# Kernel optimization log

Hardware: AMD Instinct MI355X
Metric: run time of the kernel (lower is better)

Reference implementation:

```python
import jax, jax.numpy as jnp
import numpy as np

# Coefficients expressing each of the 16 soft binary logic gates as
# c0 + ca*a + cb*b + cab*(a*b), in standard difflogic op order:
# 0:False 1:AND 2:a&~b 3:A 4:~a&b 5:B 6:XOR 7:OR 8:NOR 9:XNOR
# 10:~B 11:B=>A 12:~A 13:A=>B 14:NAND 15:True
GATE_COEF = jnp.array([
    [0, 0, 0, 0],
    [0, 0, 0, 1],
    [0, 1, 0, -1],
    [0, 1, 0, 0],
    [0, 0, 1, -1],
    [0, 0, 1, 0],
    [0, 1, 1, -2],
    [0, 1, 1, -1],
    [1, -1, -1, 1],
    [1, -1, -1, 2],
    [1, 0, -1, 0],
    [1, 0, -1, 1],
    [1, -1, 0, 0],
    [1, -1, 0, 1],
    [1, 0, 0, -1],
    [1, 0, 0, 0],
], dtype=jnp.float32)  # [16, 4]

INPUT_DIM = 8192
HIDDEN_DIMS = [16384, 16384, 16384, 16384]
OUTPUT_DIM = 1000
BATCH = 2048
TAU = 1.0
N_GATES = 16


def setup_inputs() -> dict:
    key = jax.random.key(0)
    kx, key = jax.random.split(key)
    inp = {"x": jax.random.uniform(kx, (BATCH, INPUT_DIM), dtype=jnp.float32)}
    dims = [INPUT_DIM] + HIDDEN_DIMS + [OUTPUT_DIM]
    for i in range(len(dims) - 1):
        in_d, out_d = dims[i], dims[i + 1]
        kw, ka, kb, key = jax.random.split(key, 4)
        inp[f"w{i}"] = jax.random.normal(kw, (out_d, N_GATES), dtype=jnp.float32)
        inp[f"ia{i}"] = jax.random.randint(ka, (out_d,), 0, in_d, dtype=jnp.int32)
        inp[f"ib{i}"] = jax.random.randint(kb, (out_d,), 0, in_d, dtype=jnp.int32)
    return inp


def _logic_layer(x, w, ia, ib):
    # gather the two inputs of every neuron: [batch, out_dim]
    a = x[:, ia]
    b = x[:, ib]
    p = jax.nn.softmax(w, axis=-1)              # [out_dim, 16]
    coef = p @ GATE_COEF                         # [out_dim, 4]
    # weighted mixture of all 16 gates, fused via bilinear form
    return coef[:, 0] + coef[:, 1] * a + coef[:, 2] * b + coef[:, 3] * (a * b)


def reference(x, w0, w1, w2, w3, w4, ia0, ia1, ia2, ia3, ia4, ib0, ib1, ib2, ib3, ib4):
    ws = [w0, w1, w2, w3, w4]
    ias = [ia0, ia1, ia2, ia3, ia4]
    ibs = [ib0, ib1, ib2, ib3, ib4]
    h = x
    for w, ia, ib in zip(ws, ias, ibs):
        h = _logic_layer(h, w, ia, ib)
    # GroupSum(output_dim, tau): split last dim into output_dim groups, sum, /tau
    batch = h.shape[0]
    group = h.shape[-1] // OUTPUT_DIM
    out = h.reshape(batch, OUTPUT_DIM, group).sum(-1) / TAU
    return out
```

## Files before the change

kernel.cpp:

```cpp
#include <hip/hip_runtime.h>


#define NBATCH 2048
#define IN_DIM 8192
#define HID 16384
#define OUT_DIM 1000
#define LDS_ENT 32768
#define MARKV 0x7FFFFFFF

typedef __attribute__((ext_vector_type(4))) _Float16 half4;
typedef __attribute__((ext_vector_type(2))) _Float16 half2v;

__device__ __constant__ float GC_dev[64] = {
    0, 0, 0, 0,   0, 0, 0, 1,   0, 1, 0, -1,  0, 1, 0, 0,
    0, 0, 1, -1,  0, 0, 1, 0,   0, 1, 1, -2,  0, 1, 1, -1,
    1, -1, -1, 1, 1, -1, -1, 2, 1, 0, -1, 0,  1, 0, -1, 1,
    1, -1, 0, 0,  1, -1, 0, 1,  1, 0, 0, -1,  1, 0, 0, 0
};

struct Tabs {
    const float* w[5];
    const int* ia[5];
    const int* ib[5];
};

__global__ __launch_bounds__(256) void coef_kernel(Tabs args, half4* __restrict__ coefFull) {
    int g = blockIdx.x * 256 + threadIdx.x;
    int l = g >> 14;
    int j = g & (HID - 1);
    if (l == 4 && j >= OUT_DIM) return;

    const float4* w4 = (const float4*)(args.w[l] + (size_t)j * 16);
    float v[16];
#pragma unroll
    for (int i = 0; i < 4; ++i) {
        float4 t = w4[i];
        v[4*i+0] = t.x; v[4*i+1] = t.y; v[4*i+2] = t.z; v[4*i+3] = t.w;
    }
    float m = v[0];
#pragma unroll
    for (int g2 = 1; g2 < 16; ++g2) m = fmaxf(m, v[g2]);
    float s = 0.f;
#pragma unroll
    for (int g2 = 0; g2 < 16; ++g2) { v[g2] = __expf(v[g2] - m); s += v[g2]; }
    float inv = 1.f / s;
    float c0 = 0.f, c1 = 0.f, c2 = 0.f, c3 = 0.f;
#pragma unroll
    for (int g2 = 0; g2 < 16; ++g2) {
        c0 += v[g2] * GC_dev[g2*4+0];
        c1 += v[g2] * GC_dev[g2*4+1];
        c2 += v[g2] * GC_dev[g2*4+2];
        c3 += v[g2] * GC_dev[g2*4+3];
    }
    half4 c;
    c[0] = (_Float16)(c0*inv); c[1] = (_Float16)(c1*inv);
    c[2] = (_Float16)(c2*inv); c[3] = (_Float16)(c3*inv);
    coefFull[g] = c;
}

__global__ __launch_bounds__(1024) void build_kernel(
    Tabs args, const half4* __restrict__ coefFull,
    unsigned int* __restrict__ tabIdx, half4* __restrict__ tabCoef,
    int* __restrict__ header) {
    __shared__ int mapA[HID];
    __shared__ int mapB[HID];
    __shared__ int cnt;
    const int t = threadIdx.x;

    for (int i = t; i < HID; i += 1024) mapA[i] = -1;
    if (t == 0) cnt = 0;
    __syncthreads();
    if (t < OUT_DIM) { mapA[args.ia[4][t]] = MARKV; mapA[args.ib[4][t]] = MARKV; }
    __syncthreads();
    for (int i = t; i < HID; i += 1024)
        if (mapA[i] == MARKV) mapA[i] = atomicAdd(&cnt, 1);
    __syncthreads();
    const int count3 = cnt;
    if (t < OUT_DIM) {
        unsigned a = (unsigned)(LDS_ENT - count3 + mapA[args.ia[4][t]]);
        unsigned b = (unsigned)(LDS_ENT - count3 + mapA[args.ib[4][t]]);
        tabIdx[4*HID + t] = a | (b << 16);
        tabCoef[4*HID + t] = coefFull[4*HID + t];
    }
    __syncthreads();

    for (int i = t; i < HID; i += 1024) mapB[i] = -1;
    if (t == 0) cnt = 0;
    __syncthreads();
    for (int i = t; i < HID; i += 1024)
        if (mapA[i] >= 0) { mapB[args.ia[3][i]] = MARKV; mapB[args.ib[3][i]] = MARKV; }
    __syncthreads();
    for (int i = t; i < HID; i += 1024)
        if (mapB[i] == MARKV) mapB[i] = atomicAdd(&cnt, 1);
    __syncthreads();
    const int count2 = cnt;
    for (int i = t; i < HID; i += 1024) {
        int s = mapA[i];
        if (s >= 0) {
            unsigned a = 8192u + (unsigned)mapB[args.ia[3][i]];
            unsigned b = 8192u + (unsigned)mapB[args.ib[3][i]];
            tabIdx[3*HID + s] = a | (b << 16);
            tabCoef[3*HID + s] = coefFull[3*HID + i];
        }
    }
    __syncthreads();

    for (int i = t; i < HID; i += 1024) mapA[i] = -1;
    if (t == 0) cnt = 0;
    __syncthreads();
    for (int i = t; i < HID; i += 1024)
        if (mapB[i] >= 0) { mapA[args.ia[2][i]] = MARKV; mapA[args.ib[2][i]] = MARKV; }
    __syncthreads();
    for (int i = t; i < HID; i += 1024)
        if (mapA[i] == MARKV) mapA[i] = atomicAdd(&cnt, 1);
    __syncthreads();
    const int count1 = cnt;
    {
        unsigned base1 = (unsigned)(LDS_ENT - count1);
        for (int i = t; i < HID; i += 1024) {
            int s = mapB[i];
            if (s >= 0) {
                unsigned a = base1 + (unsigned)mapA[args.ia[2][i]];
                unsigned b = base1 + (unsigned)mapA[args.ib[2][i]];
                tabIdx[2*HID + s] = a | (b << 16);
                tabCoef[2*HID + s] = coefFull[2*HID + i];
            }
        }
    }
    __syncthreads();

    for (int i = t; i < HID; i += 1024) mapB[i] = -1;
    if (t == 0) cnt = 0;
    __syncthreads();
    for (int i = t; i < HID; i += 1024)
        if (mapA[i] >= 0) { mapB[args.ia[1][i]] = MARKV; mapB[args.ib[1][i]] = MARKV; }
    __syncthreads();
    for (int i = t; i < HID; i += 1024)
        if (mapB[i] == MARKV) mapB[i] = atomicAdd(&cnt, 1);
    __syncthreads();
    const int count0 = cnt;
    for (int i = t; i < HID; i += 1024) {
        int s = mapA[i];
        if (s >= 0) {
            unsigned a = 8192u + (unsigned)mapB[args.ia[1][i]];
            unsigned b = 8192u + (unsigned)mapB[args.ib[1][i]];
            tabIdx[1*HID + s] = a | (b << 16);
            tabCoef[1*HID + s] = coefFull[1*HID + i];
        }
    }
    __syncthreads();

    for (int i = t; i < HID; i += 1024) {
        int s = mapB[i];
        if (s >= 0) {
            tabIdx[0*HID + s] =
                (unsigned)args.ia[0][i] | ((unsigned)args.ib[0][i] << 16);
            tabCoef[0*HID + s] = coefFull[0*HID + i];
        }
    }
    if (t == 0) {
        header[0] = count0; header[1] = count1;
        header[2] = count2; header[3] = count3;
    }
}

__device__ __forceinline__ void layer_pass(
    half2v* lds, const unsigned* __restrict__ tIdx,
    const half4* __restrict__ tCoef, int n, int wbase, int t) {
    for (int j = t; j < n; j += 1024) {
        unsigned idx = tIdx[j];
        half4 c = tCoef[j];
        half2v pa = lds[idx & 0xFFFFu];
        half2v pb = lds[idx >> 16];
        float c0 = (float)c[0], c1 = (float)c[1];
        float c2 = (float)c[2], c3 = (float)c[3];
        float a0 = (float)pa[0], a1 = (float)pa[1];
        float q0 = (float)pb[0], q1 = (float)pb[1];
        half2v o;
        o[0] = (_Float16)fmaf(fmaf(c3, q0, c1), a0, fmaf(c2, q0, c0));
        o[1] = (_Float16)fmaf(fmaf(c3, q1, c1), a1, fmaf(c2, q1, c0));
        lds[wbase + j] = o;
    }
    __syncthreads();
}

__global__ __launch_bounds__(1024) void fused_kernel(
    const float* __restrict__ x, const unsigned* __restrict__ tabIdx,
    const half4* __restrict__ tabCoef, const int* __restrict__ header,
    float* __restrict__ out) {
    extern __shared__ half2v lds[];
    int bp = blockIdx.x;
    int t = threadIdx.x;
    int b0 = 2 * bp, b1 = 2 * bp + 1;
    int n0 = header[0], n1 = header[1], n2 = header[2], n3 = header[3];

    const float4* xr0 = (const float4*)(x + (size_t)b0 * IN_DIM);
    const float4* xr1 = (const float4*)(x + (size_t)b1 * IN_DIM);
#pragma unroll
    for (int i = 0; i < 2; ++i) {
        int e = i * 1024 + t;
        float4 v0 = xr0[e];
        float4 v1 = xr1[e];
        half2v h0; h0[0] = (_Float16)v0.x; h0[1] = (_Float16)v1.x;
        half2v h1; h1[0] = (_Float16)v0.y; h1[1] = (_Float16)v1.y;
        half2v h2; h2[0] = (_Float16)v0.z; h2[1] = (_Float16)v1.z;
        half2v h3; h3[0] = (_Float16)v0.w; h3[1] = (_Float16)v1.w;
        lds[4*e+0] = h0; lds[4*e+1] = h1; lds[4*e+2] = h2; lds[4*e+3] = h3;
    }
    __syncthreads();

    layer_pass(lds, tabIdx + 0*HID, tabCoef + 0*HID, n0, 8192,          t);
    layer_pass(lds, tabIdx + 1*HID, tabCoef + 1*HID, n1, LDS_ENT - n1, t);
    layer_pass(lds, tabIdx + 2*HID, tabCoef + 2*HID, n2, 8192,          t);
    layer_pass(lds, tabIdx + 3*HID, tabCoef + 3*HID, n3, LDS_ENT - n3, t);

    if (t < OUT_DIM) {
        unsigned idx = tabIdx[4*HID + t];
        half4 c = tabCoef[4*HID + t];
        half2v pa = lds[idx & 0xFFFFu];
        half2v pb = lds[idx >> 16];
        float c0 = (float)c[0], c1 = (float)c[1];
        float c2 = (float)c[2], c3 = (float)c[3];
        float a0 = (float)pa[0], a1 = (float)pa[1];
        float q0 = (float)pb[0], q1 = (float)pb[1];
        out[(size_t)b0 * OUT_DIM + t] = fmaf(fmaf(c3, q0, c1), a0, fmaf(c2, q0, c0));
        out[(size_t)b1 * OUT_DIM + t] = fmaf(fmaf(c3, q1, c1), a1, fmaf(c2, q1, c0));
    }
}

extern "C" void kernel_launch(void* const* d_in, const int* in_sizes, int n_in,
                              void* d_out, int out_size, void* d_ws, size_t ws_size,
                              hipStream_t stream) {
    Tabs args;
    const float* x = (const float*)d_in[0];
    for (int i = 0; i < 5; ++i) {
        args.w[i]  = (const float*)d_in[1 + 3 * i];
        args.ia[i] = (const int*)d_in[2 + 3 * i];
        args.ib[i] = (const int*)d_in[3 + 3 * i];
    }

    char* ws = (char*)d_ws;
    half4* coefFull = (half4*)ws;
    unsigned int* tabIdx = (unsigned int*)(ws + 655360);
    half4* tabCoef = (half4*)(ws + 655360 + 327680);
    int* header = (int*)(ws + 655360 + 327680 + 655360);

    coef_kernel<<<5 * HID / 256, 256, 0, stream>>>(args, coefFull);
    build_kernel<<<1, 1024, 0, stream>>>(args, coefFull, tabIdx, tabCoef, header);
    fused_kernel<<<NBATCH / 2, 1024, LDS_ENT * sizeof(half2v), stream>>>(
        x, tabIdx, tabCoef, header, (float*)d_out);
}
```

Measured before the change: 205.2 us.

## Parallelize live-neuron pruning across many blocks and compute coefficients lazily

The single-block build kernel that walked the layers backward to find live neurons is replaced by a chain of small multi-block kernels that mark and assign compact indices through global-memory maps and atomics. Coefficient softmax is now computed only for live neurons inside the table builder, so the separate full coefficient pass is dropped. The single-workgroup serial preprocessing was the bottleneck being removed. The cost is more kernel launches and memsets, plus nondeterministic slot ordering from global atomics.

```diff
diff --git a/kernel.cpp b/kernel.cpp
--- a/kernel.cpp
+++ b/kernel.cpp
@@ -24,14 +24,9 @@
     const int* ib[5];
 };
 
-__global__ __launch_bounds__(256) void coef_kernel(Tabs args, half4* __restrict__ coefFull) {
-    int g = blockIdx.x * 256 + threadIdx.x;
-    int l = g >> 14;
-    int j = g & (HID - 1);
-    if (l == 4 && j >= OUT_DIM) return;
-
-    const float4* w4 = (const float4*)(args.w[l] + (size_t)j * 16);
+__device__ __forceinline__ half4 coef_of(const float* __restrict__ wrow) {
     float v[16];
+    const float4* w4 = (const float4*)wrow;
 #pragma unroll
     for (int i = 0; i < 4; ++i) {
         float4 t = w4[i];
@@ -39,128 +34,85 @@
     }
     float m = v[0];
 #pragma unroll
-    for (int g2 = 1; g2 < 16; ++g2) m = fmaxf(m, v[g2]);
+    for (int g = 1; g < 16; ++g) m = fmaxf(m, v[g]);
     float s = 0.f;
 #pragma unroll
-    for (int g2 = 0; g2 < 16; ++g2) { v[g2] = __expf(v[g2] - m); s += v[g2]; }
+    for (int g = 0; g < 16; ++g) { v[g] = __expf(v[g] - m); s += v[g]; }
     float inv = 1.f / s;
     float c0 = 0.f, c1 = 0.f, c2 = 0.f, c3 = 0.f;
 #pragma unroll
-    for (int g2 = 0; g2 < 16; ++g2) {
-        c0 += v[g2] * GC_dev[g2*4+0];
-        c1 += v[g2] * GC_dev[g2*4+1];
-        c2 += v[g2] * GC_dev[g2*4+2];
-        c3 += v[g2] * GC_dev[g2*4+3];
+    for (int g = 0; g < 16; ++g) {
+        c0 += v[g] * GC_dev[g*4+0];
+        c1 += v[g] * GC_dev[g*4+1];
+        c2 += v[g] * GC_dev[g*4+2];
+        c3 += v[g] * GC_dev[g*4+3];
     }
     half4 c;
     c[0] = (_Float16)(c0*inv); c[1] = (_Float16)(c1*inv);
     c[2] = (_Float16)(c2*inv); c[3] = (_Float16)(c3*inv);
-    coefFull[g] = c;
-}
-
-__global__ __launch_bounds__(1024) void build_kernel(
-    Tabs args, const half4* __restrict__ coefFull,
-    unsigned int* __restrict__ tabIdx, half4* __restrict__ tabCoef,
-    int* __restrict__ header) {
-    __shared__ int mapA[HID];
-    __shared__ int mapB[HID];
-    __shared__ int cnt;
-    const int t = threadIdx.x;
-
-    for (int i = t; i < HID; i += 1024) mapA[i] = -1;
-    if (t == 0) cnt = 0;
-    __syncthreads();
-    if (t < OUT_DIM) { mapA[args.ia[4][t]] = MARKV; mapA[args.ib[4][t]] = MARKV; }
-    __syncthreads();
-    for (int i = t; i < HID; i += 1024)
-        if (mapA[i] == MARKV) mapA[i] = atomicAdd(&cnt, 1);
-    __syncthreads();
-    const int count3 = cnt;
-    if (t < OUT_DIM) {
-        unsigned a = (unsigned)(LDS_ENT - count3 + mapA[args.ia[4][t]]);
-        unsigned b = (unsigned)(LDS_ENT - count3 + mapA[args.ib[4][t]]);
-        tabIdx[4*HID + t] = a | (b << 16);
-        tabCoef[4*HID + t] = coefFull[4*HID + t];
-    }
-    __syncthreads();
-
-    for (int i = t; i < HID; i += 1024) mapB[i] = -1;
-    if (t == 0) cnt = 0;
-    __syncthreads();
-    for (int i = t; i < HID; i += 1024)
-        if (mapA[i] >= 0) { mapB[args.ia[3][i]] = MARKV; mapB[args.ib[3][i]] = MARKV; }
-    __syncthreads();
-    for (int i = t; i < HID; i += 1024)
-        if (mapB[i] == MARKV) mapB[i] = atomicAdd(&cnt, 1);
-    __syncthreads();
-    const int count2 = cnt;
-    for (int i = t; i < HID; i += 1024) {
-        int s = mapA[i];
-        if (s >= 0) {
-            unsigned a = 8192u + (unsigned)mapB[args.ia[3][i]];
-            unsigned b = 8192u + (unsigned)mapB[args.ib[3][i]];
-            tabIdx[3*HID + s] = a | (b << 16);
-            tabCoef[3*HID + s] = coefFull[3*HID + i];
-        }
-    }
-    __syncthreads();
-
-    for (int i = t; i < HID; i += 1024) mapA[i] = -1;
-    if (t == 0) cnt = 0;
-    __syncthreads();
-    for (int i = t; i < HID; i += 1024)
-        if (mapB[i] >= 0) { mapA[args.ia[2][i]] = MARKV; mapA[args.ib[2][i]] = MARKV; }
-    __syncthreads();
-    for (int i = t; i < HID; i += 1024)
-        if (mapA[i] == MARKV) mapA[i] = atomicAdd(&cnt, 1);
-    __syncthreads();
-    const int count1 = cnt;
-    {
-        unsigned base1 = (unsigned)(LDS_ENT - count1);
-        for (int i = t; i < HID; i += 1024) {
-            int s = mapB[i];
-            if (s >= 0) {
-                unsigned a = base1 + (unsigned)mapA[args.ia[2][i]];
-                unsigned b = base1 + (unsigned)mapA[args.ib[2][i]];
-                tabIdx[2*HID + s] = a | (b << 16);
-                tabCoef[2*HID + s] = coefFull[2*HID + i];
-            }
-        }
-    }
-    __syncthreads();
-
-    for (int i = t; i < HID; i += 1024) mapB[i] = -1;
-    if (t == 0) cnt = 0;
-    __syncthreads();
-    for (int i = t; i < HID; i += 1024)
-        if (mapA[i] >= 0) { mapB[args.ia[1][i]] = MARKV; mapB[args.ib[1][i]] = MARKV; }
-    __syncthreads();
-    for (int i = t; i < HID; i += 1024)
-        if (mapB[i] == MARKV) mapB[i] = atomicAdd(&cnt, 1);
-    __syncthreads();
-    const int count0 = cnt;
-    for (int i = t; i < HID; i += 1024) {
-        int s = mapA[i];
-        if (s >= 0) {
-            unsigned a = 8192u + (unsigned)mapB[args.ia[1][i]];
-            unsigned b = 8192u + (unsigned)mapB[args.ib[1][i]];
-            tabIdx[1*HID + s] = a | (b << 16);
-            tabCoef[1*HID + s] = coefFull[1*HID + i];
-        }
-    }
-    __syncthreads();
-
-    for (int i = t; i < HID; i += 1024) {
-        int s = mapB[i];
-        if (s >= 0) {
-            tabIdx[0*HID + s] =
-                (unsigned)args.ia[0][i] | ((unsigned)args.ib[0][i] << 16);
-            tabCoef[0*HID + s] = coefFull[0*HID + i];
-        }
-    }
-    if (t == 0) {
-        header[0] = count0; header[1] = count1;
-        header[2] = count2; header[3] = count3;
+    return c;
+}
+
+__global__ __launch_bounds__(256) void mark_out_kernel(
+    const int* __restrict__ ia4, const int* __restrict__ ib4,
+    int* __restrict__ map3) {
+    int t = blockIdx.x * 256 + threadIdx.x;
+    if (t < OUT_DIM) { map3[ia4[t]] = MARKV; map3[ib4[t]] = MARKV; }
+}
+
+__global__ __launch_bounds__(256) void assign_mark_kernel(
+    int* __restrict__ mapl, int* __restrict__ mapm1,
+    const int* __restrict__ ia, const int* __restrict__ ib,
+    int* __restrict__ counter) {
+    int i = blockIdx.x * 256 + threadIdx.x;
+    if (mapl[i] == MARKV) {
+        mapl[i] = atomicAdd(counter, 1);
+        if (mapm1) { mapm1[ia[i]] = MARKV; mapm1[ib[i]] = MARKV; }
+    }
+}
+
+__global__ __launch_bounds__(256) void build_all_kernel(
+    Tabs args, const int* __restrict__ map0, const int* __restrict__ map1,
+    const int* __restrict__ map2, const int* __restrict__ map3,
+    const int* __restrict__ header,
+    unsigned int* __restrict__ tabIdx, half4* __restrict__ tabCoef) {
+    int i = blockIdx.x * 256 + threadIdx.x;
+    int n1 = header[1], n3 = header[3];
+
+    if (i < OUT_DIM) {
+        unsigned base3 = (unsigned)(LDS_ENT - n3);
+        unsigned a = base3 + (unsigned)map3[args.ia[4][i]];
+        unsigned b = base3 + (unsigned)map3[args.ib[4][i]];
+        tabIdx[4*HID + i] = a | (b << 16);
+        tabCoef[4*HID + i] = coef_of(args.w[4] + (size_t)i * 16);
+    }
+    int s3 = map3[i];
+    if (s3 >= 0) {
+        unsigned a = 8192u + (unsigned)map2[args.ia[3][i]];
+        unsigned b = 8192u + (unsigned)map2[args.ib[3][i]];
+        tabIdx[3*HID + s3] = a | (b << 16);
+        tabCoef[3*HID + s3] = coef_of(args.w[3] + (size_t)i * 16);
+    }
+    int s2 = map2[i];
+    if (s2 >= 0) {
+        unsigned base1 = (unsigned)(LDS_ENT - n1);
+        unsigned a = base1 + (unsigned)map1[args.ia[2][i]];
+        unsigned b = base1 + (unsigned)map1[args.ib[2][i]];
+        tabIdx[2*HID + s2] = a | (b << 16);
+        tabCoef[2*HID + s2] = coef_of(args.w[2] + (size_t)i * 16);
+    }
+    int s1 = map1[i];
+    if (s1 >= 0) {
+        unsigned a = 8192u + (unsigned)map0[args.ia[1][i]];
+        unsigned b = 8192u + (unsigned)map0[args.ib[1][i]];
+        tabIdx[1*HID + s1] = a | (b << 16);
+        tabCoef[1*HID + s1] = coef_of(args.w[1] + (size_t)i * 16);
+    }
+    int s0 = map0[i];
+    if (s0 >= 0) {
+        tabIdx[0*HID + s0] =
+            (unsigned)args.ia[0][i] | ((unsigned)args.ib[0][i] << 16);
+        tabCoef[0*HID + s0] = coef_of(args.w[0] + (size_t)i * 16);
     }
 }
 
@@ -209,9 +161,9 @@
     }
     __syncthreads();
 
-    layer_pass(lds, tabIdx + 0*HID, tabCoef + 0*HID, n0, 8192,          t);
+    layer_pass(lds, tabIdx + 0*HID, tabCoef + 0*HID, n0, 8192,         t);
     layer_pass(lds, tabIdx + 1*HID, tabCoef + 1*HID, n1, LDS_ENT - n1, t);
-    layer_pass(lds, tabIdx + 2*HID, tabCoef + 2*HID, n2, 8192,          t);
+    layer_pass(lds, tabIdx + 2*HID, tabCoef + 2*HID, n2, 8192,         t);
     layer_pass(lds, tabIdx + 3*HID, tabCoef + 3*HID, n3, LDS_ENT - n3, t);
 
     if (t < OUT_DIM) {
@@ -240,13 +192,27 @@
     }
 
     char* ws = (char*)d_ws;
-    half4* coefFull = (half4*)ws;
-    unsigned int* tabIdx = (unsigned int*)(ws + 655360);
-    half4* tabCoef = (half4*)(ws + 655360 + 327680);
-    int* header = (int*)(ws + 655360 + 327680 + 655360);
-
-    coef_kernel<<<5 * HID / 256, 256, 0, stream>>>(args, coefFull);
-    build_kernel<<<1, 1024, 0, stream>>>(args, coefFull, tabIdx, tabCoef, header);
+    int* maps = (int*)ws;
+    int* header = (int*)(ws + 4 * HID * 4);
+    unsigned int* tabIdx = (unsigned int*)(ws + 4*HID*4 + 64);
+    half4* tabCoef = (half4*)(ws + 4*HID*4 + 64 + 5*HID*4);
+    int* map0 = maps, *map1 = maps + HID, *map2 = maps + 2*HID, *map3 = maps + 3*HID;
+
+    hipMemsetAsync(maps, 0xFF, 4 * HID * 4, stream);
+    hipMemsetAsync(header, 0, 64, stream);
+
+    mark_out_kernel<<<(OUT_DIM + 255) / 256, 256, 0, stream>>>(
+        args.ia[4], args.ib[4], map3);
+    assign_mark_kernel<<<HID / 256, 256, 0, stream>>>(
+        map3, map2, args.ia[3], args.ib[3], header + 3);
+    assign_mark_kernel<<<HID / 256, 256, 0, stream>>>(
+        map2, map1, args.ia[2], args.ib[2], header + 2);
+    assign_mark_kernel<<<HID / 256, 256, 0, stream>>>(
+        map1, map0, args.ia[1], args.ib[1], header + 1);
+    assign_mark_kernel<<<HID / 256, 256, 0, stream>>>(
+        map0, (int*)nullptr, args.ia[0], args.ib[0], header + 0);
+    build_all_kernel<<<HID / 256, 256, 0, stream>>>(
+        args, map0, map1, map2, map3, header, tabIdx, tabCoef);
     fused_kernel<<<NBATCH / 2, 1024, LDS_ENT * sizeof(half2v), stream>>>(
         x, tabIdx, tabCoef, header, (float*)d_out);
 }
```

New measurement: 180.6 us. 1.14x faster.
